# Kernel optimization log

Hardware: AMD Instinct MI355X
Metric: run time of the kernel (lower is better)

The kernel has to match this reference:

```python
import jax, jax.numpy as jnp
import numpy as np

N, M, D = 65536, 1024, 2


def setup_inputs() -> dict:
    key = jax.random.key(0)
    k1, k2, k3 = jax.random.split(key, 3)
    sample = jax.random.uniform(k1, (N, D), dtype=jnp.float32)
    mu = jax.random.uniform(k2, (M, D), dtype=jnp.float32)
    # original init: A = 10 * I; add small noise so covariances are anisotropic
    A = 10.0 * jnp.broadcast_to(jnp.eye(D, dtype=jnp.float32), (M, D, D)) \
        + 0.1 * jax.random.normal(k3, (M, D, D), dtype=jnp.float32)
    w = jnp.ones((M, 1), dtype=jnp.float32)
    return {"sample": sample, "mu": mu, "A": A, "w": w}


def reference(sample, mu, A, w):
    # gamma_j = A_j @ A_j^T  -> precision matrices, (M, D, D)
    gamma = jnp.einsum('mde,mfe->mdf', A, A)
    # 2x2 determinant (only case implemented in the original module)
    det = gamma[:, 0, 0] * gamma[:, 1, 1] - gamma[:, 0, 1] * gamma[:, 1, 0]
    # log weights: log_softmax(w) + 0.5 * log det(gamma)
    log_w = jax.nn.log_softmax(w[:, 0], axis=0) + 0.5 * jnp.log(det)  # (M,)
    # Mahalanobis quadratic form q_ij = (x_i - mu_j)^T gamma_j (x_i - mu_j),
    # expanded to avoid materializing an (N, M, D) difference tensor.
    xGx = jnp.einsum('nd,mde,ne->nm', sample, gamma, sample)          # (N, M)
    gm = jnp.einsum('mde,me->md', gamma, mu)                          # (M, D)
    cross = sample @ gm.T                                             # (N, M)
    mGm = jnp.einsum('md,md->m', gm, mu)                              # (M,)
    q = xGx - 2.0 * cross + mGm[None, :]
    # log-likelihood per sample: logsumexp_j (log_w_j - q_ij)
    return jax.nn.logsumexp(log_w[None, :] - q, axis=1)               # (N,)
```

## Files before the change

### kernel.cpp

```cpp
#include <hip/hip_runtime.h>
#include <math.h>

#define LOG2E 1.4426950408889634f
#define LN2   0.6931471805599453f

static constexpr int M = 1024;
static constexpr int N = 65536;

typedef float v2f __attribute__((ext_vector_type(2)));

__device__ inline v2f pk_fma(v2f a, v2f b, v2f c) {
    v2f d;
    asm("v_pk_fma_f32 %0, %1, %2, %3" : "=v"(d) : "v"(a), "v"(b), "v"(c));
    return d;
}

__device__ inline float wave_max64(float v) {
    #pragma unroll
    for (int o = 32; o > 0; o >>= 1) v = fmaxf(v, __shfl_xor(v, o));
    return v;
}
__device__ inline float wave_sum64(float v) {
    #pragma unroll
    for (int o = 32; o > 0; o >>= 1) v += __shfl_xor(v, o);
    return v;
}

__global__ __launch_bounds__(1024)
void gm_prep(const float* __restrict__ mu,
             const float* __restrict__ A,
             const float* __restrict__ w,
             float* __restrict__ ws) {
    __shared__ float redA[16];
    __shared__ float redB[16];
    const int t    = threadIdx.x;
    const int lane = t & 63;
    const int wv   = t >> 6;

    const float4 a = ((const float4*)A)[t];
    const float g00 = a.x*a.x + a.y*a.y;
    const float g01 = a.x*a.z + a.y*a.w;
    const float g11 = a.z*a.z + a.w*a.w;
    const float2 m  = ((const float2*)mu)[t];
    const float gm0 = g00*m.x + g01*m.y;
    const float gm1 = g01*m.x + g11*m.y;
    const float mGm = gm0*m.x + gm1*m.y;
    const float det = g00*g11 - g01*g01;

    const float w2 = w[t] * LOG2E;
    const float t2 = w2 + 0.5f * __builtin_amdgcn_logf(det);

    float mw = wave_max64(w2);
    float mt = wave_max64(t2);
    if (lane == 0) { redA[wv] = mw; redB[wv] = mt; }
    __syncthreads();
    float wmax2 = redA[0], maxt2 = redB[0];
    #pragma unroll
    for (int i = 1; i < 16; i++) {
        wmax2 = fmaxf(wmax2, redA[i]);
        maxt2 = fmaxf(maxt2, redB[i]);
    }
    __syncthreads();
    const float sw = wave_sum64(__builtin_amdgcn_exp2f(w2 - wmax2));
    if (lane == 0) redA[wv] = sw;

    float* c = ws + (t >> 1)*12 + (t & 1);
    c[0]  = t2 - maxt2 - LOG2E * mGm;
    c[2]  = LOG2E * 2.0f * gm0;
    c[4]  = LOG2E * 2.0f * gm1;
    c[6]  = -LOG2E * g00;
    c[8]  = -LOG2E * 2.0f * g01;
    c[10] = -LOG2E * g11;

    __syncthreads();
    if (t == 0) {
        float se = 0.0f;
        #pragma unroll
        for (int i = 0; i < 16; i++) se += redA[i];
        ws[M*6] = maxt2 - (wmax2 + __builtin_amdgcn_logf(se));
    }
}

__global__ __launch_bounds__(1024, 8)
void gm_main(const float* __restrict__ sample,
             const float* __restrict__ ws,
             float* __restrict__ out) {
    __shared__ __align__(16) float coef[M*6];
    __shared__ float partial[16*128];

    const int t    = threadIdx.x;
    const int lane = t & 63;
    const int wv   = t >> 6;
    const int base = blockIdx.x * 128;

    const float2 p0 = ((const float2*)sample)[base + lane];
    const float2 p1 = ((const float2*)sample)[base + 64 + lane];

    const float k_off = ws[M*6];

    {
        const float2* src = (const float2*)ws;
        float2* dst = (float2*)coef;
        #pragma unroll
        for (int i = 0; i < 3; i++) dst[t + 1024*i] = src[t + 1024*i];
    }
    __syncthreads();

    const v2f X0  = {p0.x, p0.x},      Y0  = {p0.y, p0.y};
    const v2f XX0 = {p0.x*p0.x, p0.x*p0.x};
    const v2f XY0 = {p0.x*p0.y, p0.x*p0.y};
    const v2f YY0 = {p0.y*p0.y, p0.y*p0.y};
    const v2f X1  = {p1.x, p1.x},      Y1  = {p1.y, p1.y};
    const v2f XX1 = {p1.x*p1.x, p1.x*p1.x};
    const v2f XY1 = {p1.x*p1.y, p1.x*p1.y};
    const v2f YY1 = {p1.y*p1.y, p1.y*p1.y};

    float acc0a = 0.0f, acc0b = 0.0f, acc1a = 0.0f, acc1b = 0.0f;

    const float4* cw = (const float4*)coef + wv*32*3;
    #pragma unroll 4
    for (int jj = 0; jj < 32; jj++) {
        const float4 q0 = cw[jj*3 + 0];
        const float4 q1 = cw[jj*3 + 1];
        const float4 q2 = cw[jj*3 + 2];
        const v2f c0 = {q0.x, q0.y}, c1 = {q0.z, q0.w};
        const v2f c2 = {q1.x, q1.y}, c3 = {q1.z, q1.w};
        const v2f c4 = {q2.x, q2.y}, c5 = {q2.z, q2.w};

        v2f v0 = pk_fma(c5, YY0, pk_fma(c4, XY0, pk_fma(c3, XX0,
                 pk_fma(c2, Y0,  pk_fma(c1, X0, c0)))));
        v2f v1 = pk_fma(c5, YY1, pk_fma(c4, XY1, pk_fma(c3, XX1,
                 pk_fma(c2, Y1,  pk_fma(c1, X1, c0)))));

        acc0a += __builtin_amdgcn_exp2f(v0.x);
        acc0b += __builtin_amdgcn_exp2f(v0.y);
        acc1a += __builtin_amdgcn_exp2f(v1.x);
        acc1b += __builtin_amdgcn_exp2f(v1.y);
    }

    partial[wv*128 + lane]      = acc0a + acc0b;
    partial[wv*128 + 64 + lane] = acc1a + acc1b;
    __syncthreads();

    if (t < 128) {
        float s = partial[t];
        #pragma unroll
        for (int i = 1; i < 16; i++) s += partial[i*128 + t];
        out[base + t] = LN2 * (k_off + __builtin_amdgcn_logf(s));
    }
}

extern "C" void kernel_launch(void* const* d_in, const int* in_sizes, int n_in,
                              void* d_out, int out_size, void* d_ws, size_t ws_size,
                              hipStream_t stream) {
    const float* sample = (const float*)d_in[0];
    const float* mu     = (const float*)d_in[1];
    const float* A      = (const float*)d_in[2];
    const float* w      = (const float*)d_in[3];
    (void)in_sizes; (void)n_in; (void)out_size; (void)ws_size;

    gm_prep<<<1, 1024, 0, stream>>>(mu, A, w, (float*)d_ws);
    gm_main<<<N/128, 1024, 0, stream>>>(sample, (const float*)d_ws, (float*)d_out);
}
```

Measured before the change: 74.56 us.

## Stream mixture coefficients via double-buffered scalar loads and raise per-thread sample count

The main kernel no longer stages the 1024 component coefficients into LDS. Each wave instead takes its own 64 components and fetches them as wave-uniform data with double-buffered s_load into SGPRs, feeding packed FMAs directly from scalar operands. Each thread now evaluates 4 samples, so a block covers 256 samples and the grid is halved. The prep kernel also drops the max-shift of the log-weights, so logsumexp stability now rests on the value range of these inputs. The inline asm with manual waitcnt adds fragility in exchange for removing the LDS traffic and the block-wide barrier before compute.

```diff
diff --git a/kernel.cpp b/kernel.cpp
--- a/kernel.cpp
+++ b/kernel.cpp
@@ -7,13 +7,9 @@
 static constexpr int M = 1024;
 static constexpr int N = 65536;
 
-typedef float v2f __attribute__((ext_vector_type(2)));
-
-__device__ inline v2f pk_fma(v2f a, v2f b, v2f c) {
-    v2f d;
-    asm("v_pk_fma_f32 %0, %1, %2, %3" : "=v"(d) : "v"(a), "v"(b), "v"(c));
-    return d;
-}
+typedef float v2f  __attribute__((ext_vector_type(2)));
+typedef float v8f  __attribute__((ext_vector_type(8)));
+typedef float v16f __attribute__((ext_vector_type(16)));
 
 __device__ inline float wave_max64(float v) {
     #pragma unroll
@@ -26,13 +22,18 @@
     return v;
 }
 
+__device__ inline v2f pkfma(v2f cs, v2f f, v2f prev) {
+    v2f d;
+    asm("v_pk_fma_f32 %0, %1, %2, %3" : "=v"(d) : "s"(cs), "v"(f), "v"(prev));
+    return d;
+}
+
 __global__ __launch_bounds__(1024)
 void gm_prep(const float* __restrict__ mu,
              const float* __restrict__ A,
              const float* __restrict__ w,
              float* __restrict__ ws) {
     __shared__ float redA[16];
-    __shared__ float redB[16];
     const int t    = threadIdx.x;
     const int lane = t & 63;
     const int wv   = t >> 6;
@@ -50,103 +51,117 @@
     const float w2 = w[t] * LOG2E;
     const float t2 = w2 + 0.5f * __builtin_amdgcn_logf(det);
 
+    {
+        float* c = ws + (t >> 1)*12 + (t & 1);
+        c[0]  = t2 - LOG2E * mGm;
+        c[2]  = LOG2E * 2.0f * gm0;
+        c[4]  = LOG2E * 2.0f * gm1;
+        c[6]  = -LOG2E * g00;
+        c[8]  = -LOG2E * 2.0f * g01;
+        c[10] = -LOG2E * g11;
+    }
+
     float mw = wave_max64(w2);
-    float mt = wave_max64(t2);
-    if (lane == 0) { redA[wv] = mw; redB[wv] = mt; }
+    if (lane == 0) redA[wv] = mw;
     __syncthreads();
-    float wmax2 = redA[0], maxt2 = redB[0];
+    float wmax2 = redA[0];
     #pragma unroll
-    for (int i = 1; i < 16; i++) {
-        wmax2 = fmaxf(wmax2, redA[i]);
-        maxt2 = fmaxf(maxt2, redB[i]);
-    }
+    for (int i = 1; i < 16; i++) wmax2 = fmaxf(wmax2, redA[i]);
     __syncthreads();
     const float sw = wave_sum64(__builtin_amdgcn_exp2f(w2 - wmax2));
     if (lane == 0) redA[wv] = sw;
-
-    float* c = ws + (t >> 1)*12 + (t & 1);
-    c[0]  = t2 - maxt2 - LOG2E * mGm;
-    c[2]  = LOG2E * 2.0f * gm0;
-    c[4]  = LOG2E * 2.0f * gm1;
-    c[6]  = -LOG2E * g00;
-    c[8]  = -LOG2E * 2.0f * g01;
-    c[10] = -LOG2E * g11;
-
     __syncthreads();
     if (t == 0) {
         float se = 0.0f;
         #pragma unroll
         for (int i = 0; i < 16; i++) se += redA[i];
-        ws[M*6] = maxt2 - (wmax2 + __builtin_amdgcn_logf(se));
+        ws[M*6] = -(wmax2 + __builtin_amdgcn_logf(se));
     }
 }
 
-__global__ __launch_bounds__(1024, 8)
+__global__ __launch_bounds__(1024)
 void gm_main(const float* __restrict__ sample,
              const float* __restrict__ ws,
              float* __restrict__ out) {
-    __shared__ __align__(16) float coef[M*6];
-    __shared__ float partial[16*128];
-
+    __shared__ float partial[16*256];
     const int t    = threadIdx.x;
     const int lane = t & 63;
     const int wv   = t >> 6;
-    const int base = blockIdx.x * 128;
+    const int base = blockIdx.x * 256;
 
-    const float2 p0 = ((const float2*)sample)[base + lane];
-    const float2 p1 = ((const float2*)sample)[base + 64 + lane];
+    float xv[4], yv[4];
+    #pragma unroll
+    for (int k = 0; k < 4; ++k) {
+        const float2 p = ((const float2*)sample)[base + 64*k + lane];
+        xv[k] = p.x; yv[k] = p.y;
+    }
 
-    const float k_off = ws[M*6];
+    const int wvu = __builtin_amdgcn_readfirstlane(wv);
+    const float* cb = ws + wvu * (64*6);
 
-    {
-        const float2* src = (const float2*)ws;
-        float2* dst = (float2*)coef;
+    v2f X[4], Y[4], XX[4], XY[4], YY[4];
+    #pragma unroll
+    for (int k = 0; k < 4; ++k) {
+        X[k]  = (v2f){xv[k], xv[k]};
+        Y[k]  = (v2f){yv[k], yv[k]};
+        XX[k] = (v2f){xv[k]*xv[k], xv[k]*xv[k]};
+        XY[k] = (v2f){xv[k]*yv[k], xv[k]*yv[k]};
+        YY[k] = (v2f){yv[k]*yv[k], yv[k]*yv[k]};
+    }
+
+    float acc[4] = {0.0f, 0.0f, 0.0f, 0.0f};
+
+    v16f qA[2]; v8f qB[2];
+    asm volatile("s_load_dwordx16 %0, %1, 0"  : "=s"(qA[0]) : "s"(cb));
+    asm volatile("s_load_dwordx8  %0, %1, 64" : "=s"(qB[0]) : "s"(cb));
+
+    #pragma unroll
+    for (int b = 0; b < 16; ++b) {
+        asm volatile("s_waitcnt lgkmcnt(0)");
+        __builtin_amdgcn_sched_barrier(0);
+        if (b < 15) {
+            asm volatile("s_load_dwordx16 %0, %1, %2"
+                         : "=s"(qA[(b+1)&1]) : "s"(cb), "i"((b+1)*96));
+            asm volatile("s_load_dwordx8  %0, %1, %2"
+                         : "=s"(qB[(b+1)&1]) : "s"(cb), "i"((b+1)*96 + 64));
+        }
+        const v16f qa = qA[b&1];
+        const v8f  qb = qB[b&1];
+        const v2f c0a = {qa[0],  qa[1]},  c1a = {qa[2],  qa[3]};
+        const v2f c2a = {qa[4],  qa[5]},  c3a = {qa[6],  qa[7]};
+        const v2f c4a = {qa[8],  qa[9]},  c5a = {qa[10], qa[11]};
+        const v2f c0b = {qa[12], qa[13]}, c1b = {qa[14], qa[15]};
+        const v2f c2b = {qb[0],  qb[1]},  c3b = {qb[2],  qb[3]};
+        const v2f c4b = {qb[4],  qb[5]},  c5b = {qb[6],  qb[7]};
+
         #pragma unroll
-        for (int i = 0; i < 3; i++) dst[t + 1024*i] = src[t + 1024*i];
+        for (int k = 0; k < 4; ++k) {
+            v2f va = pkfma(c1a, X[k], c0a);
+            va = pkfma(c2a, Y[k],  va);
+            va = pkfma(c3a, XX[k], va);
+            va = pkfma(c4a, XY[k], va);
+            va = pkfma(c5a, YY[k], va);
+            v2f vb = pkfma(c1b, X[k], c0b);
+            vb = pkfma(c2b, Y[k],  vb);
+            vb = pkfma(c3b, XX[k], vb);
+            vb = pkfma(c4b, XY[k], vb);
+            vb = pkfma(c5b, YY[k], vb);
+            acc[k] += (__builtin_amdgcn_exp2f(va.x) + __builtin_amdgcn_exp2f(va.y))
+                    + (__builtin_amdgcn_exp2f(vb.x) + __builtin_amdgcn_exp2f(vb.y));
+        }
     }
+
+    #pragma unroll
+    for (int k = 0; k < 4; ++k)
+        partial[wv*256 + 64*k + lane] = acc[k];
     __syncthreads();
 
-    const v2f X0  = {p0.x, p0.x},      Y0  = {p0.y, p0.y};
-    const v2f XX0 = {p0.x*p0.x, p0.x*p0.x};
-    const v2f XY0 = {p0.x*p0.y, p0.x*p0.y};
-    const v2f YY0 = {p0.y*p0.y, p0.y*p0.y};
-    const v2f X1  = {p1.x, p1.x},      Y1  = {p1.y, p1.y};
-    const v2f XX1 = {p1.x*p1.x, p1.x*p1.x};
-    const v2f XY1 = {p1.x*p1.y, p1.x*p1.y};
-    const v2f YY1 = {p1.y*p1.y, p1.y*p1.y};
-
-    float acc0a = 0.0f, acc0b = 0.0f, acc1a = 0.0f, acc1b = 0.0f;
-
-    const float4* cw = (const float4*)coef + wv*32*3;
-    #pragma unroll 4
-    for (int jj = 0; jj < 32; jj++) {
-        const float4 q0 = cw[jj*3 + 0];
-        const float4 q1 = cw[jj*3 + 1];
-        const float4 q2 = cw[jj*3 + 2];
-        const v2f c0 = {q0.x, q0.y}, c1 = {q0.z, q0.w};
-        const v2f c2 = {q1.x, q1.y}, c3 = {q1.z, q1.w};
-        const v2f c4 = {q2.x, q2.y}, c5 = {q2.z, q2.w};
-
-        v2f v0 = pk_fma(c5, YY0, pk_fma(c4, XY0, pk_fma(c3, XX0,
-                 pk_fma(c2, Y0,  pk_fma(c1, X0, c0)))));
-        v2f v1 = pk_fma(c5, YY1, pk_fma(c4, XY1, pk_fma(c3, XX1,
-                 pk_fma(c2, Y1,  pk_fma(c1, X1, c0)))));
-
-        acc0a += __builtin_amdgcn_exp2f(v0.x);
-        acc0b += __builtin_amdgcn_exp2f(v0.y);
-        acc1a += __builtin_amdgcn_exp2f(v1.x);
-        acc1b += __builtin_amdgcn_exp2f(v1.y);
-    }
-
-    partial[wv*128 + lane]      = acc0a + acc0b;
-    partial[wv*128 + 64 + lane] = acc1a + acc1b;
-    __syncthreads();
-
-    if (t < 128) {
+    if (t < 256) {
         float s = partial[t];
         #pragma unroll
-        for (int i = 1; i < 16; i++) s += partial[i*128 + t];
-        out[base + t] = LN2 * (k_off + __builtin_amdgcn_logf(s));
+        for (int i = 1; i < 16; ++i) s += partial[i*256 + t];
+        const float nlse = ws[M*6];
+        out[base + t] = LN2 * (nlse + __builtin_amdgcn_logf(s));
     }
 }
 
@@ -160,5 +175,5 @@
     (void)in_sizes; (void)n_in; (void)out_size; (void)ws_size;
 
     gm_prep<<<1, 1024, 0, stream>>>(mu, A, w, (float*)d_ws);
-    gm_main<<<N/128, 1024, 0, stream>>>(sample, (const float*)d_ws, (float*)d_out);
+    gm_main<<<N/256, 1024, 0, stream>>>(sample, (const float*)d_ws, (float*)d_out);
 }
```

Result: no change. 75.29 us (+1.0%).
